# Optimization experiments

Measured on AMD Instinct MI355X. Metric: run time of the kernel, lower is better.

Reference implementation:

```python
import jax, jax.numpy as jnp
import numpy as np

X, Y = 128, 128           # SOM grid rows/cols
F = 512                   # num_features
B = 2048                  # batch_size
SIGMA = 1.0               # gaussian neighborhood width
LR = 0.5                  # learning rate


def setup_inputs() -> dict:
    key = jax.random.key(0)
    k1, k2 = jax.random.split(key)
    data = jax.random.normal(k1, (B, F), dtype=jnp.float32)
    # init like the module: 2*randn - 1, then L2-normalize along features
    w = 2.0 * jax.random.normal(k2, (X, Y, F), dtype=jnp.float32) - 1.0
    weights = w / jnp.linalg.norm(w, axis=-1, keepdims=True)
    return {"data": data, "weights": weights}


def reference(data, weights):
    # --- distances to all neurons (squared euclidean; argmin is sqrt-invariant) ---
    w_flat = weights.reshape(X * Y, F)                       # [XY, F]
    d2 = ((data * data).sum(-1, keepdims=True)               # [B, 1]
          + (w_flat * w_flat).sum(-1)[None, :]               # [1, XY]
          - 2.0 * jnp.einsum("bf,nf->bn", data, w_flat))    # [B, XY]
    idx = jnp.argmin(d2, axis=1)                             # [B]
    bmu_row = idx // Y
    bmu_col = idx % Y

    # --- gaussian neighborhood around each BMU on the rectangular meshgrid ---
    rows = jnp.arange(X, dtype=jnp.float32)                  # xx axis
    cols = jnp.arange(Y, dtype=jnp.float32)                  # yy axis
    dr2 = (rows[None, :] - bmu_row[:, None].astype(jnp.float32)) ** 2   # [B, X]
    dc2 = (cols[None, :] - bmu_col[:, None].astype(jnp.float32)) ** 2   # [B, Y]
    denom = 2.0 * SIGMA * SIGMA
    neigh = jnp.exp(-(dr2[:, :, None] + dc2[:, None, :]) / denom)       # [B, X, Y]

    # --- mean weighted update, without materializing [B, X, Y, F] ---
    # mean_b lr*n_b*(d_b - W) = lr*(mean_b n_b*d_b - (mean_b n_b)*W)
    nd_mean = jnp.einsum("bxy,bf->xyf", neigh, data) / B     # [X, Y, F]
    n_mean = neigh.mean(axis=0)                              # [X, Y]
    new_weights = weights + LR * (nd_mean - n_mean[:, :, None] * weights)
    return new_weights
```

## Files before the change

### kernel.cpp

```cpp
#include <hip/hip_runtime.h>


typedef __attribute__((ext_vector_type(8))) short          bf16x8;
typedef __attribute__((ext_vector_type(4))) float          f32x4;
typedef __attribute__((ext_vector_type(8))) unsigned short u16x8;

#define MFMA(a, b, c) __builtin_amdgcn_mfma_f32_16x16x32_bf16((a), (b), (c), 0, 0, 0)

static constexpr int GX = 128, GY = 128, NF = 512, NB = 2048, NXY = GX * GY;
static constexpr int RWIN = 5;
static constexpr float LR = 0.5f;

__device__ inline unsigned short f2bf(float x) {
    unsigned u = __float_as_uint(x);
    unsigned r = u + 0x7FFFu + ((u >> 16) & 1u);
    return (unsigned short)(r >> 16);
}
__device__ inline unsigned fkey(float f) {
    unsigned u = __float_as_uint(f);
    return (u & 0x80000000u) ? ~u : (u | 0x80000000u);
}
__device__ inline void glds16(const void* g, void* l) {
    __builtin_amdgcn_global_load_lds(
        (const __attribute__((address_space(1))) unsigned int*)g,
        (__attribute__((address_space(3))) unsigned int*)l, 16, 0, 0);
}

__global__ __launch_bounds__(256) void k_split(
    const float* __restrict__ A, unsigned short* __restrict__ Abf,
    const float* __restrict__ W, unsigned short* __restrict__ Wbf,
    unsigned long long* __restrict__ bmukey) {
    if (blockIdx.x == 4608) {
        int t = threadIdx.x;
#pragma unroll
        for (int j = 0; j < 8; ++j) bmukey[t * 8 + j] = ~0ull;
        return;
    }
    if (blockIdx.x < 512) {
        int i = blockIdx.x * 256 + threadIdx.x;
        const float4* a4 = (const float4*)A;
        float4 v0 = a4[2 * i], v1 = a4[2 * i + 1];
        float f[8] = {v0.x, v0.y, v0.z, v0.w, v1.x, v1.y, v1.z, v1.w};
        u16x8 h;
#pragma unroll
        for (int j = 0; j < 8; ++j) h[j] = (short)f2bf(f[j]);
        *(u16x8*)(Abf + (size_t)i * 8) = h;
    } else {
        int row  = (blockIdx.x - 512) * 4 + (threadIdx.x >> 6);
        int lane = threadIdx.x & 63;
        const float4* r4 = (const float4*)(W + (size_t)row * NF);
        float4 v0 = r4[lane * 2], v1 = r4[lane * 2 + 1];
        float f[8] = {v0.x, v0.y, v0.z, v0.w, v1.x, v1.y, v1.z, v1.w};
        u16x8 h;
#pragma unroll
        for (int j = 0; j < 8; ++j) h[j] = (short)f2bf(f[j]);
        *(u16x8*)(Wbf + (size_t)row * NF + lane * 8) = h;
    }
}

__global__ __launch_bounds__(512, 2) void k_gemm(
    const unsigned short* __restrict__ Abf, const unsigned short* __restrict__ Wbf,
    unsigned long long* __restrict__ bmukey) {
    __shared__ unsigned short lds[2][2][256 * 32];

    const int tid = threadIdx.x, lane = tid & 63, w = tid >> 6;
    const int wr = w >> 1, wc = w & 1;
    const int b = blockIdx.x;
    const int xcd = b & 7, idx = b >> 3;
    const int n0 = (((xcd << 3) | (idx & 7))) * 256;
    const int m0 = (idx >> 3) * 256;

    const int cc0 = tid, cc1 = 512 + tid;
    const int r0 = cc0 >> 2, u0 = (cc0 & 3) ^ ((r0 >> 1) & 3);
    const int r1 = cc1 >> 2, u1 = (cc1 & 3) ^ ((r1 >> 1) & 3);
    const int offA0 = (m0 + r0) * NF + u0 * 8, offA1 = (m0 + r1) * NF + u1 * 8;
    const int offB0 = (n0 + r0) * NF + u0 * 8, offB1 = (n0 + r1) * NF + u1 * 8;
    unsigned short* lbase0 = &lds[0][0][0];
    unsigned short* lbase1 = &lds[1][0][0];

#define STAGE(B, T)                                                            \
    do {                                                                       \
        const int kt_ = (T) * 32;                                              \
        unsigned short* ld_ = (B) ? lbase1 : lbase0;                           \
        glds16(Abf + offA0 + kt_, ld_ + cc0 * 8);                              \
        glds16(Abf + offA1 + kt_, ld_ + cc1 * 8);                              \
        glds16(Wbf + offB0 + kt_, ld_ + 8192 + cc0 * 8);                       \
        glds16(Wbf + offB1 + kt_, ld_ + 8192 + cc1 * 8);                       \
    } while (0)

    int aoff[4], boff[8];
#pragma unroll
    for (int m = 0; m < 4; ++m) {
        int row = wr * 64 + m * 16 + (lane & 15);
        int s   = (lane >> 4) ^ ((row >> 1) & 3);
        aoff[m] = row * 32 + s * 8;
    }
#pragma unroll
    for (int n = 0; n < 8; ++n) {
        int row = wc * 128 + n * 16 + (lane & 15);
        int s   = (lane >> 4) ^ ((row >> 1) & 3);
        boff[n] = 8192 + row * 32 + s * 8;
    }

    f32x4 acc[4][8];
#pragma unroll
    for (int m = 0; m < 4; ++m)
#pragma unroll
        for (int n = 0; n < 8; ++n) acc[m][n] = (f32x4){0.f, 0.f, 0.f, 0.f};

#define COMPUTE(B)                                                             \
    do {                                                                       \
        unsigned short* lb_ = (B) ? lbase1 : lbase0;                           \
        bf16x8 af[4], bf[4];                                                   \
        _Pragma("unroll") for (int m = 0; m < 4; ++m)                          \
            af[m] = *(const bf16x8*)(lb_ + aoff[m]);                           \
        _Pragma("unroll") for (int n = 0; n < 4; ++n)                          \
            bf[n] = *(const bf16x8*)(lb_ + boff[n]);                           \
        __builtin_amdgcn_s_setprio(1);                                         \
        _Pragma("unroll") for (int n = 0; n < 4; ++n)                          \
            _Pragma("unroll") for (int m = 0; m < 4; ++m)                      \
                acc[m][n] = MFMA(af[m], bf[n], acc[m][n]);                     \
        __builtin_amdgcn_s_setprio(0);                                         \
        _Pragma("unroll") for (int n = 0; n < 4; ++n)                          \
            bf[n] = *(const bf16x8*)(lb_ + boff[n + 4]);                       \
        __builtin_amdgcn_s_setprio(1);                                         \
        _Pragma("unroll") for (int n = 0; n < 4; ++n)                          \
            _Pragma("unroll") for (int m = 0; m < 4; ++m)                      \
                acc[m][n + 4] = MFMA(af[m], bf[n], acc[m][n + 4]);             \
        __builtin_amdgcn_s_setprio(0);                                         \
    } while (0)

    STAGE(0, 0);
    __syncthreads();
#pragma unroll 1
    for (int t = 0; t < 16; t += 2) {
        if (t + 1 < 16) STAGE(1, t + 1);
        COMPUTE(0);
        __syncthreads();
        if (t + 2 < 16) STAGE(0, t + 2);
        COMPUTE(1);
        __syncthreads();
    }

#pragma unroll
    for (int m = 0; m < 4; ++m)
#pragma unroll
        for (int reg = 0; reg < 4; ++reg) {
            int grow = m0 + wr * 64 + m * 16 + (lane >> 4) * 4 + reg;
            unsigned long long key = ~0ull;
#pragma unroll
            for (int n = 0; n < 8; ++n) {
                unsigned long long k2 =
                    ((unsigned long long)fkey(-acc[m][n][reg]) << 32) |
                    (unsigned)(n0 + wc * 128 + n * 16 + (lane & 15));
                key = (k2 < key) ? k2 : key;
            }
#pragma unroll
            for (int mask = 1; mask <= 8; mask <<= 1) {
                unsigned long long o = __shfl_xor(key, mask);
                key = (o < key) ? o : key;
            }
            if ((lane & 15) == 0) atomicMin(bmukey + grow, key);
        }
#undef STAGE
#undef COMPUTE
}

__global__ __launch_bounds__(1024) void k_bin(
    const unsigned long long* __restrict__ bmukey,
    int* __restrict__ counts, int* __restrict__ offsets,
    int* __restrict__ cinfo, int* __restrict__ occ_cell,
    int* __restrict__ n_occ, int* __restrict__ list) {
    __shared__ int sbmu[NB];
    __shared__ int scnt[NXY];
    __shared__ int soff[NXY];
    __shared__ int ws[16], wo[16];
    const int t = threadIdx.x, lane = t & 63, w = t >> 6;

    for (int i = t; i < NXY; i += 1024) scnt[i] = 0;
    for (int i = t; i < NB; i += 1024) sbmu[i] = (int)(bmukey[i] & 0xFFFFFFFFull);
    __syncthreads();
    for (int i = t; i < NB; i += 1024) atomicAdd(&scnt[sbmu[i]], 1);
    __syncthreads();

    const int base = t * 16;
    int sc = 0, so = 0;
#pragma unroll
    for (int i = 0; i < 16; ++i) { int c = scnt[base + i]; sc += c; so += (c != 0); }
    int vs = sc, vo = so;
#pragma unroll
    for (int d = 1; d < 64; d <<= 1) {
        int us = __shfl_up(vs, d), uo = __shfl_up(vo, d);
        if (lane >= d) { vs += us; vo += uo; }
    }
    if (lane == 63) { ws[w] = vs; wo[w] = vo; }
    __syncthreads();
    if (t == 0) {
        int rs = 0, ro = 0;
        for (int i = 0; i < 16; ++i) {
            int a = ws[i]; ws[i] = rs; rs += a;
            int c = wo[i]; wo[i] = ro; ro += c;
        }
        n_occ[0] = ro;
    }
    __syncthreads();
    int es = vs - sc + ws[w];
    int eo = vo - so + wo[w];
    for (int i = 0; i < 16; ++i) {
        int cell = base + i, c = scnt[cell];
        soff[cell] = es;
        offsets[cell] = es;
        cinfo[cell] = (c << 16) | eo;
        counts[cell] = c;
        if (c) { occ_cell[eo] = cell; eo++; }
        es += c;
    }
    __syncthreads();

    if (w == 0) {
        for (int g = 0; g < 32; ++g) {
            int bb = g * 64 + lane;
            int key = sbmu[bb];
            unsigned long long match = ~0ull;
#pragma unroll
            for (int j = 0; j < 14; ++j) {
                unsigned long long bj = __ballot((key >> j) & 1);
                match &= ((key >> j) & 1) ? bj : ~bj;
            }
            unsigned long long below = ((unsigned long long)1 << lane) - 1;
            int rin = __popcll(match & below);
            int bse = soff[key];
            if (rin == 0) soff[key] = bse + __popcll(match);
            list[bse + rin] = bb;
        }
    }
}

__global__ __launch_bounds__(256) void k_gc(const float* __restrict__ data,
                                            const int* __restrict__ counts,
                                            const int* __restrict__ offsets,
                                            const int* __restrict__ list,
                                            const int* __restrict__ occ_cell,
                                            const int* __restrict__ n_occ,
                                            float* __restrict__ Gc) {
    int s = blockIdx.x;
    if (s >= n_occ[0]) return;
    int cell = occ_cell[s];
    int cnt = counts[cell], off = offsets[cell];
    int t = threadIdx.x;
    float ax = 0.f, ay = 0.f;
    for (int i = 0; i < cnt; ++i) {
        int b = list[off + i];
        float2 d = ((const float2*)data)[b * 256 + t];
        ax += d.x;
        ay += d.y;
    }
    float2 g = {ax, ay};
    ((float2*)Gc)[(size_t)s * 256 + t] = g;
}

__global__ __launch_bounds__(256) void k_update(
    const float* __restrict__ W, const float* __restrict__ Gc,
    const int* __restrict__ cinfo, float* __restrict__ out) {
    __shared__ int sslot[200];
    __shared__ float srow[200], srowcnt[200];
    __shared__ int sbyd[200];
    __shared__ float swf[1600], swfc[1600];
    __shared__ float nwt8[8];
    __shared__ int wcnt[4];
    const int x = blockIdx.x >> 4, y0 = (blockIdx.x & 15) << 3;
    const int t = threadIdx.x, w = t >> 6, lane = t & 63;

    bool valid = false;
    float rowfac = 0.f;
    int slot = 0, cnt = 0, byd = 0;
    if (t < 198) {
        int bx = x - RWIN + t / 18;
        int by = y0 - RWIN + t % 18;
        if ((unsigned)bx < 128u && (unsigned)by < 128u) {
            int info = cinfo[(bx << 7) | by];
            if (info > 0xFFFF) {
                valid = true;
                cnt = info >> 16;
                slot = info & 0xFFFF;
                int dx = x - bx;
                rowfac = __expf(-0.5f * (float)(dx * dx));
                byd = by - y0;
            }
        }
    }
    unsigned long long m = __ballot(valid);
    int rin = __popcll(m & (((unsigned long long)1 << lane) - 1ull));
    if (lane == 0) wcnt[w] = __popcll(m);
    __syncthreads();
    int pre = 0;
    for (int i = 0; i < w; ++i) pre += wcnt[i];
    if (valid) {
        int pos = pre + rin;
        sslot[pos] = slot;
        srow[pos] = rowfac;
        srowcnt[pos] = rowfac * (float)cnt;
        sbyd[pos] = byd;
    }
    __syncthreads();
    const int ne = wcnt[0] + wcnt[1] + wcnt[2] + wcnt[3];

    for (int idx = t; idx < ne * 8; idx += 256) {
        int e = idx >> 3, o = idx & 7;
        int d = sbyd[e] - o;
        float cf = ((unsigned)(d + RWIN) <= 2u * RWIN)
                       ? __expf(-0.5f * (float)(d * d)) : 0.f;
        swf[idx] = srow[e] * cf;
        swfc[idx] = srowcnt[e] * cf;
    }
    __syncthreads();
    if (t < 8) {
        float s = 0.f;
        for (int e = 0; e < ne; ++e) s += swfc[e * 8 + t];
        nwt8[t] = s;
    }
    __syncthreads();

    float2 acc[8];
#pragma unroll
    for (int o = 0; o < 8; ++o) acc[o] = (float2){0.f, 0.f};
    const float2* gc2 = (const float2*)Gc;
    for (int e = 0; e < ne; ++e) {
        float2 g = gc2[sslot[e] * 256 + t];
#pragma unroll
        for (int o = 0; o < 8; ++o) {
            float f = swf[e * 8 + o];
            acc[o].x += f * g.x;
            acc[o].y += f * g.y;
        }
    }

    const float c = LR / (float)NB;
    const float2* W2 = (const float2*)W;
    float2* O2 = (float2*)out;
#pragma unroll
    for (int o = 0; o < 8; ++o) {
        size_t n = (size_t)((x << 7) | (y0 + o));
        float2 w2 = W2[n * 256 + t];
        float nw = nwt8[o];
        float2 r;
        r.x = w2.x + c * (acc[o].x - nw * w2.x);
        r.y = w2.y + c * (acc[o].y - nw * w2.y);
        O2[n * 256 + t] = r;
    }
}

extern "C" void kernel_launch(void* const* d_in, const int* in_sizes, int n_in,
                              void* d_out, int out_size, void* d_ws, size_t ws_size,
                              hipStream_t stream) {
    const float* data = (const float*)d_in[0];
    const float* W    = (const float*)d_in[1];
    float* out = (float*)d_out;
    char* ws = (char*)d_ws;

    unsigned short* Abf = (unsigned short*)(ws + 0);
    float*          Gc  = (float*)(ws + 0);
    unsigned long long* bmukey = (unsigned long long*)(ws + 4259840);
    int* counts   = (int*)(ws + 4276224);
    int* offsets  = (int*)(ws + 4341760);
    int* cinfo    = (int*)(ws + 4407296);
    int* occ_cell = (int*)(ws + 4472832);
    int* list     = (int*)(ws + 4481024);
    int* n_occ    = (int*)(ws + 4489216);

    unsigned short* Wbf = (unsigned short*)d_out;

    k_split<<<4609, 256, 0, stream>>>(data, Abf, W, Wbf, bmukey);

    k_gemm<<<512, 512, 0, stream>>>(Abf, Wbf, bmukey);

    k_bin<<<1, 1024, 0, stream>>>(bmukey, counts, offsets, cinfo, occ_cell,
                                  n_occ, list);
    k_gc<<<NB, 256, 0, stream>>>(data, counts, offsets, list, occ_cell, n_occ, Gc);
    k_update<<<2048, 256, 0, stream>>>(W, Gc, cinfo, out);
}
```

Baseline: 130.9 us.

## Split A/B tile staging and interleave with MFMA phases using explicit waitcnts

Restructures the BMU distance GEMM main loop: A and W tiles are staged separately, with the W tile for step t+1 issued during step t and the A tile for t+2 issued into the current buffer once its A fragments are held in registers. Full __syncthreads are replaced with raw s_barrier, manual vmcnt/lgkmcnt waits and sched_barriers, so global loads stay in flight across MFMA blocks instead of draining at every barrier. This adds more barriers per iteration and depends on hand-tuned wait counts being correct, which risks races on the shared LDS buffers.

```diff
diff --git a/kernel.cpp b/kernel.cpp
--- a/kernel.cpp
+++ b/kernel.cpp
@@ -78,15 +78,21 @@
     unsigned short* lbase0 = &lds[0][0][0];
     unsigned short* lbase1 = &lds[1][0][0];
 
-#define STAGE(B, T)                                                            \
+#define STAGE_A(LD, KT)                                                        \
     do {                                                                       \
-        const int kt_ = (T) * 32;                                              \
-        unsigned short* ld_ = (B) ? lbase1 : lbase0;                           \
-        glds16(Abf + offA0 + kt_, ld_ + cc0 * 8);                              \
-        glds16(Abf + offA1 + kt_, ld_ + cc1 * 8);                              \
-        glds16(Wbf + offB0 + kt_, ld_ + 8192 + cc0 * 8);                       \
-        glds16(Wbf + offB1 + kt_, ld_ + 8192 + cc1 * 8);                       \
+        glds16(Abf + offA0 + (KT), (LD) + cc0 * 8);                            \
+        glds16(Abf + offA1 + (KT), (LD) + cc1 * 8);                            \
     } while (0)
+#define STAGE_B(LD, KT)                                                        \
+    do {                                                                       \
+        glds16(Wbf + offB0 + (KT), (LD) + 8192 + cc0 * 8);                     \
+        glds16(Wbf + offB1 + (KT), (LD) + 8192 + cc1 * 8);                     \
+    } while (0)
+#define SBAR()   __builtin_amdgcn_s_barrier()
+#define SCHEDB() __builtin_amdgcn_sched_barrier(0)
+#define WAITL0() asm volatile("s_waitcnt lgkmcnt(0)" ::: "memory")
+#define WAITV2() asm volatile("s_waitcnt vmcnt(2)" ::: "memory")
+#define WAITV0() asm volatile("s_waitcnt vmcnt(0)" ::: "memory")
 
     int aoff[4], boff[8];
 #pragma unroll
@@ -108,38 +114,51 @@
 #pragma unroll
         for (int n = 0; n < 8; ++n) acc[m][n] = (f32x4){0.f, 0.f, 0.f, 0.f};
 
-#define COMPUTE(B)                                                             \
-    do {                                                                       \
-        unsigned short* lb_ = (B) ? lbase1 : lbase0;                           \
-        bf16x8 af[4], bf[4];                                                   \
-        _Pragma("unroll") for (int m = 0; m < 4; ++m)                          \
-            af[m] = *(const bf16x8*)(lb_ + aoff[m]);                           \
-        _Pragma("unroll") for (int n = 0; n < 4; ++n)                          \
-            bf[n] = *(const bf16x8*)(lb_ + boff[n]);                           \
-        __builtin_amdgcn_s_setprio(1);                                         \
-        _Pragma("unroll") for (int n = 0; n < 4; ++n)                          \
-            _Pragma("unroll") for (int m = 0; m < 4; ++m)                      \
-                acc[m][n] = MFMA(af[m], bf[n], acc[m][n]);                     \
-        __builtin_amdgcn_s_setprio(0);                                         \
-        _Pragma("unroll") for (int n = 0; n < 4; ++n)                          \
-            bf[n] = *(const bf16x8*)(lb_ + boff[n + 4]);                       \
-        __builtin_amdgcn_s_setprio(1);                                         \
-        _Pragma("unroll") for (int n = 0; n < 4; ++n)                          \
-            _Pragma("unroll") for (int m = 0; m < 4; ++m)                      \
-                acc[m][n + 4] = MFMA(af[m], bf[n], acc[m][n + 4]);             \
-        __builtin_amdgcn_s_setprio(0);                                         \
-    } while (0)
-
-    STAGE(0, 0);
-    __syncthreads();
+    STAGE_A(lbase0, 0);
+    STAGE_B(lbase0, 0);
+    STAGE_A(lbase1, 32);
+    WAITV2();
+    SCHEDB();
+    SBAR();
+    SCHEDB();
+
 #pragma unroll 1
-    for (int t = 0; t < 16; t += 2) {
-        if (t + 1 < 16) STAGE(1, t + 1);
-        COMPUTE(0);
-        __syncthreads();
-        if (t + 2 < 16) STAGE(0, t + 2);
-        COMPUTE(1);
-        __syncthreads();
+    for (int t = 0; t < 16; ++t) {
+        unsigned short* cb = (t & 1) ? lbase1 : lbase0;
+        unsigned short* nb = (t & 1) ? lbase0 : lbase1;
+        const int kt1 = (t + 1) * 32, kt2 = (t + 2) * 32;
+        bf16x8 af[4], bf[4];
+#pragma unroll
+        for (int m = 0; m < 4; ++m) af[m] = *(const bf16x8*)(cb + aoff[m]);
+#pragma unroll
+        for (int n = 0; n < 4; ++n) bf[n] = *(const bf16x8*)(cb + boff[n]);
+        if (t < 15) STAGE_B(nb, kt1);
+        SBAR(); WAITL0(); SCHEDB();
+        __builtin_amdgcn_s_setprio(1);
+#pragma unroll
+        for (int n = 0; n < 4; ++n)
+#pragma unroll
+            for (int m = 0; m < 4; ++m)
+                acc[m][n] = MFMA(af[m], bf[n], acc[m][n]);
+        __builtin_amdgcn_s_setprio(0);
+        SCHEDB(); SBAR(); SCHEDB();
+#pragma unroll
+        for (int n = 0; n < 4; ++n) bf[n] = *(const bf16x8*)(cb + boff[n + 4]);
+        if (t < 14) STAGE_A(cb, kt2);
+        SBAR(); WAITL0(); SCHEDB();
+        __builtin_amdgcn_s_setprio(1);
+#pragma unroll
+        for (int n = 0; n < 4; ++n)
+#pragma unroll
+            for (int m = 0; m < 4; ++m)
+                acc[m][n + 4] = MFMA(af[m], bf[n], acc[m][n + 4]);
+        __builtin_amdgcn_s_setprio(0);
+        if (t < 14) {
+            WAITV2();
+        } else if (t == 14) {
+            WAITV0();
+        }
+        SCHEDB(); SBAR(); SCHEDB();
     }
 
 #pragma unroll
@@ -162,8 +181,13 @@
             }
             if ((lane & 15) == 0) atomicMin(bmukey + grow, key);
         }
-#undef STAGE
-#undef COMPUTE
+#undef STAGE_A
+#undef STAGE_B
+#undef SBAR
+#undef SCHEDB
+#undef WAITL0
+#undef WAITV2
+#undef WAITV0
 }
 
 __global__ __launch_bounds__(1024) void k_bin(
```

Measured after the change: 132.7 us. About the same (+1.4%).
